# Kernel tuning notes

Measured on AMD Instinct MI355X. Metric: run time of the kernel, lower is better.

Reference implementation:

```python
import jax, jax.numpy as jnp
import numpy as np

ALPHA = 0.2  # LeakyReLU negative slope


def setup_inputs() -> dict:
    key = jax.random.key(0)
    ks = jax.random.split(key, 8)
    E, R, F = 2048, 24, 128
    return {
        "ent_mat": jax.random.normal(ks[0], (E, F), jnp.float32),
        "rel_mat": jax.random.normal(ks[1], (R, F), jnp.float32),
        "adjacencies": jax.random.uniform(ks[2], (R, E, E), jnp.float32),
        "A": jax.random.uniform(ks[3], (E, R), jnp.float32),
        "weight_ent": jax.random.normal(ks[4], (F, F), jnp.float32) / np.sqrt(F).astype(np.float32),
        "weight_rel": jax.random.normal(ks[5], (F, F), jnp.float32) / np.sqrt(F).astype(np.float32),
        "lin_w": jax.random.normal(ks[6], (F,), jnp.float32) / np.sqrt(F).astype(np.float32),
        "lin_b": jax.random.normal(ks[7], (1,), jnp.float32) * 0.01,
    }


def reference(ent_mat, rel_mat, adjacencies, A, weight_ent, weight_rel, lin_w, lin_b):
    E, F = ent_mat.shape
    R = rel_mat.shape[0]
    # per-relation message aggregation: spmm(adj_r, ent_mat) for each r -> [R, E, F]
    supports = jnp.einsum('rij,jf->rif', adjacencies, ent_mat)

    # ---- RelatEntAtt (concat=False, eval mode -> dropout is identity) ----
    adj = jax.nn.softmax(A, axis=1)                         # [E, R]
    a_input = ent_mat[:, None, :] * rel_mat[None, :, :]     # [E, R, F] outer product h_e * r_r
    att = jax.nn.leaky_relu(adj[:, :, None] * a_input, negative_slope=ALPHA)  # [E, R, F]
    att_E = jax.nn.softmax(att, axis=0)                     # softmax over entities
    att_R = jax.nn.softmax(att, axis=1)                     # softmax over relations
    # linear(att_R): [E, R, 1]; torch .view(R, E, -1) is a raw row-major reshape
    alpha = (jnp.einsum('erf,f->er', att_R, lin_w) + lin_b[0]).reshape(R, E, 1)
    alpha = jax.nn.softmax(alpha, axis=1)                   # softmax over E
    h_prime = jnp.sum(att_E * ent_mat[:, None, :], axis=1)  # [E, F]
    r_prime = jnp.sum(att_R * rel_mat[None, :, :], axis=0)  # [R, F]

    # ---- combine ----
    ent_output = h_prime + jnp.sum(supports * alpha, axis=0) @ weight_ent  # [E, F]
    rel_output = r_prime @ weight_rel                                      # [R, F]
    return ent_output, rel_output
```

## Files before the change

kernel.cpp:

```cpp
#include <hip/hip_runtime.h>
#include <math.h>

#define E 2048
#define R 24
#define F 128
#define NSLOPE 0.2f
#define CH 32
#define ECH (E/CH)
#define PIN 12

typedef unsigned short ushort_t;
typedef unsigned int uint_t;
typedef __attribute__((ext_vector_type(8))) short bf16x8;
typedef __attribute__((ext_vector_type(4))) float f32x4;

__device__ __forceinline__ float lrelu(float x){ return x>0.f ? x : NSLOPE*x; }
__device__ __forceinline__ ushort_t f2bf(float f){
  uint_t u = __float_as_uint(f);
  u += 0x7FFF + ((u>>16)&1);
  return (ushort_t)(u>>16);
}

__global__ __launch_bounds__(128) void k_phaseA(const float* __restrict__ A,
    const float* __restrict__ ent, const float* __restrict__ rel,
    const float* __restrict__ linw, const float* __restrict__ linb,
    float* __restrict__ psum, float* __restrict__ alin){
  int bid = blockIdx.x;
  int f = threadIdx.x;
  if (bid < R*CH){
    __shared__ float sm[ECH];
    int r = bid >> 5, c = bid & 31;
    int e0 = c*ECH;
    if (f < ECH){
      int e = e0 + f;
      float sum = 0.f, mine = 0.f;
      #pragma unroll
      for (int q=0;q<R;++q){
        float x = __expf(A[e*R+q]);
        sum += x; if (q==r) mine = x;
      }
      sm[f] = mine/sum;
    }
    __syncthreads();
    float relv = rel[r*F+f];
    float s = 0.f;
    for (int e=e0; e<e0+ECH; ++e)
      s += __expf(lrelu(sm[e-e0]*ent[e*F+f]*relv));
    psum[(r*CH+c)*F+f] = s;
  } else {
    int e0 = (bid - R*CH)*4;
    int lane = f&63, w = f>>6;
    __shared__ float part[2][R];
    float relv[R];
    #pragma unroll
    for (int r=0;r<R;++r) relv[r] = rel[r*F+f];
    float lw = linw[f], lb = linb[0];
    for (int e=e0; e<e0+4; ++e){
      float av[R]; float as = 0.f;
      #pragma unroll
      for (int q=0;q<R;++q){ av[q] = __expf(A[e*R+q]); as += av[q]; }
      float ainv = 1.f/as;
      float entv = ent[e*F+f];
      float ex[R]; float rs = 0.f;
      #pragma unroll
      for (int r=0;r<R;++r){ float x = __expf(lrelu(av[r]*ainv*entv*relv[r])); ex[r]=x; rs+=x; }
      float invrs = 1.f/rs;
      float c[R];
      #pragma unroll
      for (int r=0;r<R;++r) c[r] = ex[r]*invrs*lw;
      #pragma unroll
      for (int off=32; off>=1; off>>=1){
        #pragma unroll
        for (int r=0;r<R;++r) c[r] += __shfl_xor(c[r], off);
      }
      if (lane==0){
        #pragma unroll
        for (int r=0;r<R;++r) part[w][r] = c[r];
      }
      __syncthreads();
      if (f < R) alin[e*R+f] = part[0][f] + part[1][f] + lb;
      __syncthreads();
    }
  }
}

__global__ __launch_bounds__(256) void k_phaseB(const float* __restrict__ psum,
    const float* __restrict__ alin, const float* __restrict__ A,
    float* __restrict__ colinv, float* __restrict__ srow,
    float* __restrict__ alpha, float* __restrict__ adj_smT){
  int bid = blockIdx.x, t = threadIdx.x;
  if (bid < R){
    __shared__ float red[256];
    int r = bid;
    float v[8]; float m = -1e30f;
    #pragma unroll
    for (int i=0;i<8;++i){ v[i] = alin[r*E + i*256 + t]; m = fmaxf(m, v[i]); }
    red[t] = m; __syncthreads();
    for (int s=128; s>0; s>>=1){ if (t<s) red[t] = fmaxf(red[t], red[t+s]); __syncthreads(); }
    m = red[0]; __syncthreads();
    float sum = 0.f;
    #pragma unroll
    for (int i=0;i<8;++i){ v[i] = __expf(v[i]-m); sum += v[i]; }
    red[t] = sum; __syncthreads();
    for (int s=128; s>0; s>>=1){ if (t<s) red[t] += red[t+s]; __syncthreads(); }
    float inv = 1.f/red[0];
    #pragma unroll
    for (int i=0;i<8;++i) alpha[r*E + i*256 + t] = v[i]*inv;
  } else if (bid < R+12){
    int idx = (bid-R)*256 + t;
    int r = idx / F, ff = idx % F;
    float S = 0.f;
    #pragma unroll
    for (int c=0;c<CH;++c) S += psum[(r*CH+c)*F+ff];
    colinv[idx] = 1.f/S;
    srow[idx] = 0.f;
  } else {
    int e = (bid-R-12)*256 + t;
    float av[R]; float as = 0.f;
    #pragma unroll
    for (int q=0;q<R;++q){ av[q] = __expf(A[e*R+q]); as += av[q]; }
    float ainv = 1.f/as;
    #pragma unroll
    for (int q=0;q<R;++q) adj_smT[q*E+e] = av[q]*ainv;
  }
}

__global__ __launch_bounds__(256) void k_big(const float* __restrict__ adj,
    const float* __restrict__ alpha, const float* __restrict__ adj_smT,
    const float* __restrict__ ent, const float* __restrict__ rel,
    const float* __restrict__ colinv, const float* __restrict__ went,
    ushort_t* __restrict__ Bbf, float* __restrict__ out_h,
    float* __restrict__ srow, ushort_t* __restrict__ W2T){
  int bid = blockIdx.x, t = threadIdx.x;
  if (bid < E){
    int lane = t&63, w = t>>6, e = bid;
    const f32x4* a4 = (const f32x4*)adj;
    int i0 = w*128 + lane;
    f32x4 acc0 = {0.f,0.f,0.f,0.f};
    f32x4 acc1 = {0.f,0.f,0.f,0.f};
    #pragma unroll 6
    for (int r=0; r<PIN; ++r){
      float al = alpha[r*E + e];
      const f32x4* p = a4 + (((size_t)r*E + e) << 9) + i0;
      f32x4 v0 = p[0];
      f32x4 v1 = p[64];
      acc0 += al*v0; acc1 += al*v1;
    }
    #pragma unroll 6
    for (int r=PIN; r<R; ++r){
      float al = alpha[r*E + e];
      const f32x4* p = a4 + (((size_t)r*E + e) << 9) + i0;
      f32x4 v0 = __builtin_nontemporal_load(p);
      f32x4 v1 = __builtin_nontemporal_load(p + 64);
      acc0 += al*v0; acc1 += al*v1;
    }
    ushort4 o0, o1;
    o0.x = f2bf(acc0.x); o0.y = f2bf(acc0.y); o0.z = f2bf(acc0.z); o0.w = f2bf(acc0.w);
    o1.x = f2bf(acc1.x); o1.y = f2bf(acc1.y); o1.z = f2bf(acc1.z); o1.w = f2bf(acc1.w);
    ushort_t* brow = Bbf + (size_t)e*E;
    *(ushort4*)(brow + (size_t)i0*4)      = o0;
    *(ushort4*)(brow + (size_t)(i0+64)*4) = o1;
  } else if (bid < E+512){
    if (t >= 128) return;
    int f = t; int e0 = (bid-E)*4;
    float relv[R], ci[R], sR[R];
    #pragma unroll
    for (int r=0;r<R;++r){ relv[r]=rel[r*F+f]; ci[r]=colinv[r*F+f]; sR[r]=0.f; }
    for (int e=e0; e<e0+4; ++e){
      float entv = ent[e*F+f];
      float rs = 0.f, sumE = 0.f;
      #pragma unroll
      for (int r=0;r<R;++r){
        float x = __expf(lrelu(adj_smT[r*E+e]*entv*relv[r]));
        rs += x; sumE += x*ci[r];
      }
      float invrs = 1.f/rs;
      #pragma unroll
      for (int r=0;r<R;++r){
        float x = __expf(lrelu(adj_smT[r*E+e]*entv*relv[r]));
        sR[r] += x*invrs;
      }
      out_h[e*F+f] = entv*sumE;
    }
    #pragma unroll
    for (int r=0;r<R;++r) atomicAdd(&srow[r*F+f], sR[r]);
  } else {
    if (t >= 128) return;
    int fo = t; int e0 = (bid-E-512)*8;
    float acc[8];
    #pragma unroll
    for (int k=0;k<8;++k) acc[k]=0.f;
    for (int fi=0; fi<F; ++fi){
      float wv = went[fi*F+fo];
      #pragma unroll
      for (int k=0;k<8;++k) acc[k] += ent[(e0+k)*F+fi]*wv;
    }
    #pragma unroll
    for (int k=0;k<8;++k) W2T[(size_t)fo*E + e0 + k] = f2bf(acc[k]);
  }
}

__global__ __launch_bounds__(512) void k_phaseD(const ushort_t* __restrict__ Bbf,
    const ushort_t* __restrict__ W2T, const float* __restrict__ rel,
    const float* __restrict__ srow, const float* __restrict__ wrel,
    float* __restrict__ out){
  int bid = blockIdx.x, tt = threadIdx.x;
  if (bid < 2*(E/16)){
    int l = tt & 63, w = tt >> 6;
    int m16 = (bid >> 1) << 4;
    int kh  = bid & 1;
    int n16 = w << 4;
    const bf16x8* ap = (const bf16x8*)(Bbf + (size_t)(m16 + (l & 15))*E + kh*(E/2) + ((l >> 4)*8));
    const bf16x8* bp = (const bf16x8*)(W2T + (size_t)(n16 + (l & 15))*E + kh*(E/2) + ((l >> 4)*8));
    f32x4 acc = {0.f,0.f,0.f,0.f};
    #pragma unroll 4
    for (int k=0; k<E/64; ++k){
      bf16x8 av = ap[k*4];
      bf16x8 bv = bp[k*4];
      acc = __builtin_amdgcn_mfma_f32_16x16x32_bf16(av, bv, acc, 0, 0, 0);
    }
    int row = m16 + (l >> 4)*4;
    int col = n16 + (l & 15);
    #pragma unroll
    for (int v=0; v<4; ++v)
      atomicAdd(&out[(size_t)(row+v)*F + col], acc[v]);
  } else {
    if (tt >= 128) return;
    int fo = tt; int r = bid - 2*(E/16);
    float acc = 0.f;
    for (int fi=0; fi<F; ++fi) acc += rel[r*F+fi]*srow[r*F+fi]*wrel[fi*F+fo];
    out[E*F + r*F + fo] = acc;
  }
}

extern "C" void kernel_launch(void* const* d_in, const int* in_sizes, int n_in,
                              void* d_out, int out_size, void* d_ws, size_t ws_size,
                              hipStream_t stream) {
  const float* ent  = (const float*)d_in[0];
  const float* rel  = (const float*)d_in[1];
  const float* adj  = (const float*)d_in[2];
  const float* A    = (const float*)d_in[3];
  const float* went = (const float*)d_in[4];
  const float* wrel = (const float*)d_in[5];
  const float* linw = (const float*)d_in[6];
  const float* linb = (const float*)d_in[7];
  float* out = (float*)d_out;

  float* ws = (float*)d_ws;
  float* psum    = ws;
  float* colinv  = psum + R*CH*F;
  float* srow    = colinv + R*F;
  float* alin    = srow + R*F;
  float* alpha   = alin + E*R;
  float* adj_smT = alpha + E*R;
  ushort_t* W2T  = (ushort_t*)(adj_smT + R*E);
  ushort_t* Bbf  = W2T + (size_t)F*E;

  k_phaseA<<<dim3(R*CH + 512), dim3(128), 0, stream>>>(A, ent, rel, linw, linb, psum, alin);
  k_phaseB<<<dim3(R + 12 + 8), dim3(256), 0, stream>>>(psum, alin, A, colinv, srow, alpha, adj_smT);
  k_big<<<dim3(E + 512 + 256), dim3(256), 0, stream>>>(adj, alpha, adj_smT, ent, rel, colinv,
                                                       went, Bbf, out, srow, W2T);
  k_phaseD<<<dim3(2*(E/16) + R), dim3(512), 0, stream>>>(Bbf, W2T, rel, srow, wrel, out);
}
```

Measured before the change: 121.7 us.

## Split streaming kernel from attention work, cache exps, and quarter-split GEMM K

Splits the fused k_big kernel into a pure streaming kernel (with an occupancy hint) and a separate 128-thread kernel for the attention and ent@W work, so half-idle 256-thread blocks no longer share the launch. The attention path now stores the per-relation exponentials in registers instead of recomputing them. The final bf16 MFMA GEMM splits K into four parts instead of two, giving more blocks but twice as many atomic adds to the output. It adds one extra kernel launch and runs the small work serially after the stream instead of overlapping with it.

```diff
diff --git a/kernel.cpp b/kernel.cpp
--- a/kernel.cpp
+++ b/kernel.cpp
@@ -125,68 +125,65 @@
   }
 }
 
-__global__ __launch_bounds__(256) void k_big(const float* __restrict__ adj,
-    const float* __restrict__ alpha, const float* __restrict__ adj_smT,
+__global__ __launch_bounds__(256, 8) void k_stream(const float* __restrict__ adj,
+    const float* __restrict__ alpha, ushort_t* __restrict__ Bbf){
+  int t = threadIdx.x;
+  int lane = t&63, w = t>>6, e = blockIdx.x;
+  const f32x4* a4 = (const f32x4*)adj;
+  int i0 = w*128 + lane;
+  f32x4 acc0 = {0.f,0.f,0.f,0.f};
+  f32x4 acc1 = {0.f,0.f,0.f,0.f};
+  #pragma unroll 6
+  for (int r=0; r<PIN; ++r){
+    float al = alpha[r*E + e];
+    const f32x4* p = a4 + (((size_t)r*E + e) << 9) + i0;
+    f32x4 v0 = p[0];
+    f32x4 v1 = p[64];
+    acc0 += al*v0; acc1 += al*v1;
+  }
+  #pragma unroll 6
+  for (int r=PIN; r<R; ++r){
+    float al = alpha[r*E + e];
+    const f32x4* p = a4 + (((size_t)r*E + e) << 9) + i0;
+    f32x4 v0 = __builtin_nontemporal_load(p);
+    f32x4 v1 = __builtin_nontemporal_load(p + 64);
+    acc0 += al*v0; acc1 += al*v1;
+  }
+  ushort4 o0, o1;
+  o0.x = f2bf(acc0.x); o0.y = f2bf(acc0.y); o0.z = f2bf(acc0.z); o0.w = f2bf(acc0.w);
+  o1.x = f2bf(acc1.x); o1.y = f2bf(acc1.y); o1.z = f2bf(acc1.z); o1.w = f2bf(acc1.w);
+  ushort_t* brow = Bbf + (size_t)e*E;
+  *(ushort4*)(brow + (size_t)i0*4)      = o0;
+  *(ushort4*)(brow + (size_t)(i0+64)*4) = o1;
+}
+
+__global__ __launch_bounds__(128) void k_finish(const float* __restrict__ adj_smT,
     const float* __restrict__ ent, const float* __restrict__ rel,
     const float* __restrict__ colinv, const float* __restrict__ went,
-    ushort_t* __restrict__ Bbf, float* __restrict__ out_h,
-    float* __restrict__ srow, ushort_t* __restrict__ W2T){
+    float* __restrict__ out_h, float* __restrict__ srow, ushort_t* __restrict__ W2T){
   int bid = blockIdx.x, t = threadIdx.x;
-  if (bid < E){
-    int lane = t&63, w = t>>6, e = bid;
-    const f32x4* a4 = (const f32x4*)adj;
-    int i0 = w*128 + lane;
-    f32x4 acc0 = {0.f,0.f,0.f,0.f};
-    f32x4 acc1 = {0.f,0.f,0.f,0.f};
-    #pragma unroll 6
-    for (int r=0; r<PIN; ++r){
-      float al = alpha[r*E + e];
-      const f32x4* p = a4 + (((size_t)r*E + e) << 9) + i0;
-      f32x4 v0 = p[0];
-      f32x4 v1 = p[64];
-      acc0 += al*v0; acc1 += al*v1;
-    }
-    #pragma unroll 6
-    for (int r=PIN; r<R; ++r){
-      float al = alpha[r*E + e];
-      const f32x4* p = a4 + (((size_t)r*E + e) << 9) + i0;
-      f32x4 v0 = __builtin_nontemporal_load(p);
-      f32x4 v1 = __builtin_nontemporal_load(p + 64);
-      acc0 += al*v0; acc1 += al*v1;
-    }
-    ushort4 o0, o1;
-    o0.x = f2bf(acc0.x); o0.y = f2bf(acc0.y); o0.z = f2bf(acc0.z); o0.w = f2bf(acc0.w);
-    o1.x = f2bf(acc1.x); o1.y = f2bf(acc1.y); o1.z = f2bf(acc1.z); o1.w = f2bf(acc1.w);
-    ushort_t* brow = Bbf + (size_t)e*E;
-    *(ushort4*)(brow + (size_t)i0*4)      = o0;
-    *(ushort4*)(brow + (size_t)(i0+64)*4) = o1;
-  } else if (bid < E+512){
-    if (t >= 128) return;
-    int f = t; int e0 = (bid-E)*4;
+  if (bid < 512){
+    int f = t; int e0 = bid*4;
     float relv[R], ci[R], sR[R];
     #pragma unroll
     for (int r=0;r<R;++r){ relv[r]=rel[r*F+f]; ci[r]=colinv[r*F+f]; sR[r]=0.f; }
     for (int e=e0; e<e0+4; ++e){
       float entv = ent[e*F+f];
-      float rs = 0.f, sumE = 0.f;
+      float ex[R]; float rs = 0.f, sumE = 0.f;
       #pragma unroll
       for (int r=0;r<R;++r){
         float x = __expf(lrelu(adj_smT[r*E+e]*entv*relv[r]));
-        rs += x; sumE += x*ci[r];
+        ex[r] = x; rs += x; sumE += x*ci[r];
       }
       float invrs = 1.f/rs;
       #pragma unroll
-      for (int r=0;r<R;++r){
-        float x = __expf(lrelu(adj_smT[r*E+e]*entv*relv[r]));
-        sR[r] += x*invrs;
-      }
+      for (int r=0;r<R;++r) sR[r] += ex[r]*invrs;
       out_h[e*F+f] = entv*sumE;
     }
     #pragma unroll
     for (int r=0;r<R;++r) atomicAdd(&srow[r*F+f], sR[r]);
   } else {
-    if (t >= 128) return;
-    int fo = t; int e0 = (bid-E-512)*8;
+    int fo = t; int e0 = (bid-512)*8;
     float acc[8];
     #pragma unroll
     for (int k=0;k<8;++k) acc[k]=0.f;
@@ -205,16 +202,16 @@
     const float* __restrict__ srow, const float* __restrict__ wrel,
     float* __restrict__ out){
   int bid = blockIdx.x, tt = threadIdx.x;
-  if (bid < 2*(E/16)){
+  if (bid < 4*(E/16)){
     int l = tt & 63, w = tt >> 6;
-    int m16 = (bid >> 1) << 4;
-    int kh  = bid & 1;
+    int m16 = (bid >> 2) << 4;
+    int kq  = bid & 3;
     int n16 = w << 4;
-    const bf16x8* ap = (const bf16x8*)(Bbf + (size_t)(m16 + (l & 15))*E + kh*(E/2) + ((l >> 4)*8));
-    const bf16x8* bp = (const bf16x8*)(W2T + (size_t)(n16 + (l & 15))*E + kh*(E/2) + ((l >> 4)*8));
+    const bf16x8* ap = (const bf16x8*)(Bbf + (size_t)(m16 + (l & 15))*E + kq*(E/4) + ((l >> 4)*8));
+    const bf16x8* bp = (const bf16x8*)(W2T + (size_t)(n16 + (l & 15))*E + kq*(E/4) + ((l >> 4)*8));
     f32x4 acc = {0.f,0.f,0.f,0.f};
     #pragma unroll 4
-    for (int k=0; k<E/64; ++k){
+    for (int k=0; k<E/128; ++k){
       bf16x8 av = ap[k*4];
       bf16x8 bv = bp[k*4];
       acc = __builtin_amdgcn_mfma_f32_16x16x32_bf16(av, bv, acc, 0, 0, 0);
@@ -226,7 +223,7 @@
       atomicAdd(&out[(size_t)(row+v)*F + col], acc[v]);
   } else {
     if (tt >= 128) return;
-    int fo = tt; int r = bid - 2*(E/16);
+    int fo = tt; int r = bid - 4*(E/16);
     float acc = 0.f;
     for (int fi=0; fi<F; ++fi) acc += rel[r*F+fi]*srow[r*F+fi]*wrel[fi*F+fo];
     out[E*F + r*F + fo] = acc;
@@ -258,7 +255,8 @@
 
   k_phaseA<<<dim3(R*CH + 512), dim3(128), 0, stream>>>(A, ent, rel, linw, linb, psum, alin);
   k_phaseB<<<dim3(R + 12 + 8), dim3(256), 0, stream>>>(psum, alin, A, colinv, srow, alpha, adj_smT);
-  k_big<<<dim3(E + 512 + 256), dim3(256), 0, stream>>>(adj, alpha, adj_smT, ent, rel, colinv,
-                                                       went, Bbf, out, srow, W2T);
-  k_phaseD<<<dim3(2*(E/16) + R), dim3(512), 0, stream>>>(Bbf, W2T, rel, srow, wrel, out);
-}
+  k_stream<<<dim3(E), dim3(256), 0, stream>>>(adj, alpha, Bbf);
+  k_finish<<<dim3(512 + 256), dim3(128), 0, stream>>>(adj_smT, ent, rel, colinv, went,
+                                                      out, srow, W2T);
+  k_phaseD<<<dim3(4*(E/16) + R), dim3(512), 0, stream>>>(Bbf, W2T, rel, srow, wrel, out);
+}
```

Measured after the change: 137.6 us. +13.1%, slower.
